# Kernel tuning notes

Measured on AMD Instinct MI355X. Metric: run time of the kernel, lower is better.

## Reference

```python
import jax, jax.numpy as jnp
import numpy as np

B, R, T, D = 16, 1024, 512, 1024
H = 1024  # hidden_dim

def setup_inputs() -> dict:
    key = jax.random.key(0)
    ks = jax.random.split(key, 8)
    s_in = 1.0 / np.sqrt(D)
    s_comb = 1.0 / np.sqrt(3 * D)
    return {
        "region_feats": jax.random.normal(ks[0], (B, R, D), jnp.float32),
        "query_embs": jax.random.normal(ks[1], (B, T, D), jnp.float32),
        "Wr": jax.random.normal(ks[2], (D, H), jnp.float32) * s_in,
        "br": jnp.zeros((H,), jnp.float32),
        "Wq": jax.random.normal(ks[3], (D, H), jnp.float32) * s_in,
        "bq": jnp.zeros((H,), jnp.float32),
        "Ws": jax.random.normal(ks[4], (3 * D, 1), jnp.float32) * s_comb,
        "bs": jnp.zeros((1,), jnp.float32),
    }

def reference(region_feats, query_embs, Wr, br, Wq, bq, Ws, bs):
    # Dense projections
    R_proj = region_feats @ Wr + br            # [B,R,H]
    Q_proj = query_embs @ Wq + bq              # [B,T,H]
    # Unscaled cross-attention scores
    scores = jnp.einsum('brd,btd->brt', R_proj, Q_proj)  # [B,R,T]
    attn = jax.nn.softmax(scores, axis=-1)
    # Attend over RAW query embeddings (as in source)
    attended = jnp.einsum('brt,btd->brd', attn, query_embs)  # [B,R,D]
    combined = jnp.concatenate(
        [region_feats, attended, region_feats * attended], axis=-1)  # [B,R,3D]
    out = combined @ Ws + bs                    # [B,R,1]
    return jnp.squeeze(out, axis=-1)            # [B,R]
```

## Files before the change

kernel.cpp:

```cpp
#include <hip/hip_runtime.h>


#define BD 16
#define RD 1024
#define TD 512
#define DD 1024
#define BR (BD * RD)

typedef _Float16 half8 __attribute__((ext_vector_type(8)));
typedef _Float16 half4 __attribute__((ext_vector_type(4)));
typedef float floatx4 __attribute__((ext_vector_type(4)));

__device__ __forceinline__ float wave_sum(float v) {
#pragma unroll
  for (int off = 32; off > 0; off >>= 1) v += __shfl_down(v, off);
  return v;
}

__device__ __forceinline__ half8 cvt8(float4 a, float4 b) {
  half8 h = {(_Float16)a.x, (_Float16)a.y, (_Float16)a.z, (_Float16)a.w,
             (_Float16)b.x, (_Float16)b.y, (_Float16)b.z, (_Float16)b.w};
  return h;
}

__device__ __forceinline__ void gl16(const _Float16* g, _Float16* l) {
  __builtin_amdgcn_global_load_lds(
      (const __attribute__((address_space(1))) void*)g,
      (__attribute__((address_space(3))) void*)l, 16, 0, 0);
}

#define VMW_(N) asm volatile("s_waitcnt vmcnt(" #N ")" ::: "memory")
#define VMW(N) VMW_(N)
#define BARR                        \
  __builtin_amdgcn_s_barrier();     \
  asm volatile("" ::: "memory")

__global__ __launch_bounds__(256) void prep_all(
    const float* __restrict__ Wr, const float* __restrict__ Wq,
    const float* __restrict__ Ws, const float* __restrict__ br,
    const float* __restrict__ region, const float* __restrict__ query,
    _Float16* __restrict__ M2, _Float16* __restrict__ Ws16,
    float* __restrict__ wqbr, _Float16* __restrict__ wqbr16,
    _Float16* __restrict__ r16, float* __restrict__ rdvec,
    _Float16* __restrict__ q16, float* __restrict__ h1) {
  __shared__ __align__(16) _Float16 lds[2 * 2 * 2048];
  const int blk = blockIdx.x, tid = threadIdx.x;

  if (blk < 256) {
    const int m0 = (blk >> 4) * 64, n0 = (blk & 15) * 64;
    const int lane = tid & 63, w = tid >> 6;
    const int wr = w >> 1, wc = w & 1;
    const int srow = tid >> 2, slot = tid & 3;
    const int scol = (slot ^ ((srow >> 1) & 3)) * 8;
    const long offA = (long)(m0 + srow) * DD + scol;
    const long offB = (long)(n0 + srow) * DD + scol;
    const int wofs = srow * 32 + slot * 8;
    const int NK = DD / 32;
    float4 a0, a1, b0, b1;
    a0 = *(const float4*)(Wr + offA); a1 = *(const float4*)(Wr + offA + 4);
    b0 = *(const float4*)(Wq + offB); b1 = *(const float4*)(Wq + offB + 4);
    *(int4*)&lds[wofs] = *(int4*)&(const half8&)cvt8(a0, a1);
    {
      half8 hb = cvt8(b0, b1);
      *(half8*)&lds[2048 + wofs] = hb;
    }
    a0 = *(const float4*)(Wr + offA + 32); a1 = *(const float4*)(Wr + offA + 36);
    b0 = *(const float4*)(Wq + offB + 32); b1 = *(const float4*)(Wq + offB + 36);
    __syncthreads();
    floatx4 acc[2][2] = {};
    const int fr = lane & 15, g = lane >> 4;
    const int fs = (g ^ ((fr >> 1) & 3)) * 8;
    for (int kt = 0; kt < NK; ++kt) {
      const int cur = (kt & 1) * 4096, nxt = ((kt + 1) & 1) * 4096;
      if (kt + 1 < NK) {
        half8 ha = cvt8(a0, a1), hb = cvt8(b0, b1);
        *(half8*)&lds[nxt + wofs] = ha;
        *(half8*)&lds[nxt + 2048 + wofs] = hb;
      }
      if (kt + 2 < NK) {
        const long go = (long)(kt + 2) * 32;
        a0 = *(const float4*)(Wr + offA + go); a1 = *(const float4*)(Wr + offA + go + 4);
        b0 = *(const float4*)(Wq + offB + go); b1 = *(const float4*)(Wq + offB + go + 4);
      }
      half8 af[2], bf[2];
#pragma unroll
      for (int i = 0; i < 2; ++i)
        af[i] = *(const half8*)&lds[cur + (32 * wr + 16 * i + fr) * 32 + fs];
#pragma unroll
      for (int j = 0; j < 2; ++j)
        bf[j] = *(const half8*)&lds[cur + 2048 + (32 * wc + 16 * j + fr) * 32 + fs];
#pragma unroll
      for (int i = 0; i < 2; ++i)
#pragma unroll
        for (int j = 0; j < 2; ++j)
          acc[i][j] = __builtin_amdgcn_mfma_f32_16x16x32_f16(af[i], bf[j], acc[i][j], 0, 0, 0);
      __syncthreads();
    }
    const int cr = g * 4, cc = fr;
#pragma unroll
    for (int i = 0; i < 2; ++i)
#pragma unroll
      for (int r = 0; r < 4; ++r)
#pragma unroll
        for (int j = 0; j < 2; ++j)
          M2[(long)(m0 + 32 * wr + 16 * i + cr + r) * DD + n0 + 32 * wc + 16 * j + cc] =
              (_Float16)acc[i][j][r];
  } else if (blk < 258) {
    const long i = (long)(blk - 256) * 1024 + tid * 4;
    const float4 v = *(const float4*)&Ws[DD + i];
    half4 h = {(_Float16)v.x, (_Float16)v.y, (_Float16)v.z, (_Float16)v.w};
    *(half4*)&Ws16[i] = h;
  } else if (blk < 514) {
    const int row = (blk - 258) * 4 + (tid >> 6);
    const int lane = tid & 63;
    const float* x = Wq + (long)row * DD;
    float s = 0.f;
    for (int k = lane; k < DD; k += 64) s += x[k] * br[k];
    s = wave_sum(s);
    if (lane == 0) {
      wqbr[row] = s;
      wqbr16[row] = (_Float16)s;
    }
  } else if (blk < 514 + BR / 4) {
    const int wid = tid >> 6, lane = tid & 63;
    const long row = (long)(blk - 514) * 4 + wid;
    const float* src = region + row * DD;
    _Float16* dst = r16 + row * DD;
    float rd = 0.f;
#pragma unroll
    for (int it = 0; it < 4; ++it) {
      const int c = it * 256 + lane * 4;
      const float4 v = *(const float4*)&src[c];
      const float4 w0 = *(const float4*)&Ws[c];
      half4 h = {(_Float16)v.x, (_Float16)v.y, (_Float16)v.z, (_Float16)v.w};
      *(half4*)&dst[c] = h;
      rd += v.x * w0.x + v.y * w0.y + v.z * w0.z + v.w * w0.w;
    }
    rd = wave_sum(rd);
    if (lane == 0) rdvec[row] = rd;
  } else {
    const int wid = tid >> 6, lane = tid & 63;
    const long row = (long)(blk - (514 + BR / 4)) * 4 + wid;
    const float* src = query + row * DD;
    _Float16* dst = q16 + row * DD;
    float hq = 0.f;
#pragma unroll
    for (int it = 0; it < 4; ++it) {
      const int c = it * 256 + lane * 4;
      const float4 v = *(const float4*)&src[c];
      const float4 w1 = *(const float4*)&Ws[DD + c];
      half4 h = {(_Float16)v.x, (_Float16)v.y, (_Float16)v.z, (_Float16)v.w};
      *(half4*)&dst[c] = h;
      hq += v.x * w1.x + v.y * w1.y + v.z * w1.z + v.w * w1.w;
    }
    hq = wave_sum(hq);
    if (lane == 0) h1[row] = hq;
  }
}

#define STAGE2(hh, sl)                                  \
  {                                                     \
    const long go_ = (long)(hh) * 32;                   \
    gl16(gA + go_, &lds[(sl) * 8192 + wbase]);          \
    gl16(gB + go_, &lds[(sl) * 8192 + 4096 + wbase]);   \
  }

#define COMP2(h, sl)                                                           \
  {                                                                            \
    half8 af[2], bf[4];                                                        \
    _Pragma("unroll") for (int i = 0; i < 2; ++i)                              \
      af[i] = *(const half8*)&lds[(sl) * 8192 + (32 * wr + 16 * i + fr) * 32 + fs]; \
    _Pragma("unroll") for (int j = 0; j < 4; ++j)                              \
      bf[j] = *(const half8*)&lds[(sl) * 8192 + 4096 + (64 * wc + 16 * j + fr) * 32 + fs]; \
    if (wc == 0) {                                                             \
      const half8 wb = *(const half8*)&wq_lds[(h) * 32 + g * 8];               \
      _Pragma("unroll") for (int i = 0; i < 2; ++i)                            \
        _Pragma("unroll") for (int e = 0; e < 8; ++e)                          \
          cvp[i] += (float)af[i][e] * (float)wb[e];                            \
    }                                                                          \
    __builtin_amdgcn_s_setprio(1);                                             \
    _Pragma("unroll") for (int i = 0; i < 2; ++i)                              \
      _Pragma("unroll") for (int j = 0; j < 4; ++j)                            \
        acc[i][j] = __builtin_amdgcn_mfma_f32_16x16x32_f16(af[i], bf[j], acc[i][j], 0, 0, 0); \
    __builtin_amdgcn_s_setprio(0);                                             \
  }

__global__ __launch_bounds__(512, 4) void qp_gemm(
    const _Float16* __restrict__ A, const _Float16* __restrict__ B,
    _Float16* __restrict__ C, const _Float16* __restrict__ wq16,
    float* __restrict__ cvec) {
  __shared__ __align__(16) _Float16 lds[4 * 8192];
  __shared__ __align__(16) _Float16 wq_lds[1024];
  const int lin = blockIdx.x;
  const int s = lin & 7, u = lin >> 3;
  const int mt = s * 8 + (u >> 3), nt = u & 7;
  const int m0 = mt * 128, n0 = nt * 128;
  const int tid = threadIdx.x, lane = tid & 63, w = tid >> 6;
  const int wr = w >> 1, wc = w & 1;

  const int lrow = lane >> 2, slot = lane & 3;
  const int scol = (slot ^ ((lrow >> 1) & 3)) * 8;
  const int srow = 16 * w + lrow;
  const _Float16* gA = A + (long)(m0 + srow) * DD + scol;
  const _Float16* gB = B + (long)(n0 + srow) * DD + scol;
  const int wbase = 512 * w;

  if (tid < 128) *(int4*)&wq_lds[tid * 8] = *(const int4*)&wq16[tid * 8];
  __syncthreads();

  floatx4 acc[2][4] = {};
  float cvp[2] = {0.f, 0.f};
  const int fr = lane & 15, g = lane >> 4;
  const int fs = (g ^ ((fr >> 1) & 3)) * 8;

  STAGE2(0, 0); STAGE2(1, 1); STAGE2(2, 2);
  VMW(4); BARR;

  for (int hb = 0; hb < 28; hb += 4) {
    STAGE2(hb + 3, 3); COMP2(hb + 0, 0); VMW(4); BARR;
    STAGE2(hb + 4, 0); COMP2(hb + 1, 1); VMW(4); BARR;
    STAGE2(hb + 5, 1); COMP2(hb + 2, 2); VMW(4); BARR;
    STAGE2(hb + 6, 2); COMP2(hb + 3, 3); VMW(4); BARR;
  }
  STAGE2(31, 3); COMP2(28, 0); VMW(4); BARR;
  COMP2(29, 1); VMW(2); BARR;
  COMP2(30, 2); VMW(0); BARR;
  COMP2(31, 3);

  if (wc == 0 && nt == 0) {
#pragma unroll
    for (int i = 0; i < 2; ++i) {
      float c = cvp[i];
      c += __shfl_xor(c, 16);
      c += __shfl_xor(c, 32);
      if (lane < 16) cvec[m0 + 32 * wr + 16 * i + lane] = c;
    }
  }

  const int cr = g * 4, cc = fr;
#pragma unroll
  for (int i = 0; i < 2; ++i)
#pragma unroll
    for (int r = 0; r < 4; ++r)
#pragma unroll
      for (int j = 0; j < 4; ++j)
        C[(long)(m0 + 32 * wr + 16 * i + cr + r) * DD + n0 + 64 * wc + 16 * j + cc] =
            (_Float16)acc[i][j][r];
}

__global__ __launch_bounds__(512, 4) void gemm_fused(
    const _Float16* __restrict__ A, const _Float16* __restrict__ B0,
    const _Float16* __restrict__ B1,
    float* __restrict__ Ms, float* __restrict__ Ls, float* __restrict__ Hs,
    const float* __restrict__ cvec, const float* __restrict__ h1,
    const _Float16* __restrict__ wsh, long sA, long sB) {
  __shared__ __align__(16) _Float16 lds[2 * 3 * 4096];
  __shared__ __align__(16) _Float16 wlds[1024];

  const int lin = blockIdx.x;
  const int s = lin & 7, u = lin >> 3;
  const int b = 2 * s + (u >> 5);
  const int t = u & 31;
  const int mt = t >> 2, nt = t & 3;
  const int m0 = mt * 128, n0 = nt * 128;
  A += (long)b * sA;
  B0 += (long)b * sB;
  B1 += (long)b * sB;

  const int tid = threadIdx.x, lane = tid & 63, w = tid >> 6;
  const int wr = w >> 2, wc = w & 3;

  const int lrow = lane >> 2, slot = lane & 3;
  const int scol = (slot ^ ((lrow >> 1) & 3)) * 8;
  const int srow = 16 * w + lrow;
  const _Float16* gA = A + (long)(m0 + srow) * DD + scol;
  const _Float16* gP = B0 + (long)(n0 + srow) * DD + scol;
  const _Float16* gQ = B1 + (long)(n0 + srow) * DD + scol;
  const int wbase = 512 * w;

  if (tid < 128) *(int4*)&wlds[tid * 8] = *(const int4*)&wsh[1024 + tid * 8];

  gl16(gA, &lds[wbase]);
  gl16(gP, &lds[4096 + wbase]);
  gl16(gQ, &lds[8192 + wbase]);
  __syncthreads();

  floatx4 accS[4][2] = {};
  floatx4 accH[4][2] = {};
  const int fr = lane & 15, g = lane >> 4;
  const int fs = (g ^ ((fr >> 1) & 3)) * 8;
  const int NK = DD / 32;

  for (int kt = 0; kt < NK; ++kt) {
    const int cur = (kt & 1) * 12288;
    const int nxt = cur ^ 12288;
    if (kt + 1 < NK) {
      const long go = (long)(kt + 1) * 32;
      gl16(gA + go, &lds[nxt + wbase]);
      gl16(gP + go, &lds[nxt + 4096 + wbase]);
      gl16(gQ + go, &lds[nxt + 8192 + wbase]);
    }
    half8 af[4], bp[2], bq[2];
#pragma unroll
    for (int i = 0; i < 4; ++i)
      af[i] = *(const half8*)&lds[cur + (64 * wr + 16 * i + fr) * 32 + fs];
#pragma unroll
    for (int j = 0; j < 2; ++j)
      bp[j] = *(const half8*)&lds[cur + 4096 + (32 * wc + 16 * j + fr) * 32 + fs];
#pragma unroll
    for (int j = 0; j < 2; ++j)
      bq[j] = *(const half8*)&lds[cur + 8192 + (32 * wc + 16 * j + fr) * 32 + fs];
    const half8 w2f = *(const half8*)&wlds[kt * 32 + g * 8];
#pragma unroll
    for (int j = 0; j < 2; ++j) bq[j] *= w2f;
#pragma unroll
    for (int i = 0; i < 4; ++i)
#pragma unroll
      for (int j = 0; j < 2; ++j)
        accS[i][j] = __builtin_amdgcn_mfma_f32_16x16x32_f16(af[i], bp[j], accS[i][j], 0, 0, 0);
#pragma unroll
    for (int i = 0; i < 4; ++i)
#pragma unroll
      for (int j = 0; j < 2; ++j)
        accH[i][j] = __builtin_amdgcn_mfma_f32_16x16x32_f16(af[i], bq[j], accH[i][j], 0, 0, 0);
    __syncthreads();
  }

  const int cr = g * 4, cc = fr;
  float cv[2], hv[2];
#pragma unroll
  for (int j = 0; j < 2; ++j) {
    const long col = (long)b * TD + n0 + 32 * wc + 16 * j + cc;
    cv[j] = cvec[col];
    hv[j] = h1[col];
  }

  float* smx = (float*)(void*)lds;
  float* slv = smx + 512;
  float* shv = slv + 512;
#pragma unroll
  for (int i = 0; i < 4; ++i) {
#pragma unroll
    for (int r = 0; r < 4; ++r) {
      float mx = fmaxf(accS[i][0][r] + cv[0], accS[i][1][r] + cv[1]);
      mx = fmaxf(mx, __shfl_xor(mx, 1));
      mx = fmaxf(mx, __shfl_xor(mx, 2));
      mx = fmaxf(mx, __shfl_xor(mx, 4));
      mx = fmaxf(mx, __shfl_xor(mx, 8));
      float l = 0.f, hs = 0.f;
#pragma unroll
      for (int j = 0; j < 2; ++j) {
        const float e = __expf(accS[i][j][r] + cv[j] - mx);
        l += e;
        hs += e * (accH[i][j][r] + hv[j]);
      }
      l += __shfl_xor(l, 1); hs += __shfl_xor(hs, 1);
      l += __shfl_xor(l, 2); hs += __shfl_xor(hs, 2);
      l += __shfl_xor(l, 4); hs += __shfl_xor(hs, 4);
      l += __shfl_xor(l, 8); hs += __shfl_xor(hs, 8);
      if (cc == 0) {
        const int rw = 16 * i + cr + r;
        smx[wr * 256 + wc * 64 + rw] = mx;
        slv[wr * 256 + wc * 64 + rw] = l;
        shv[wr * 256 + wc * 64 + rw] = hs;
      }
    }
  }
  __syncthreads();
  if (tid < 128) {
    const int rw = tid & 63, w2 = tid >> 6;
    float m4[4], gm = -1e30f;
#pragma unroll
    for (int c = 0; c < 4; ++c) {
      m4[c] = smx[w2 * 256 + c * 64 + rw];
      gm = fmaxf(gm, m4[c]);
    }
    float L = 0.f, H = 0.f;
#pragma unroll
    for (int c = 0; c < 4; ++c) {
      const float sc = __expf(m4[c] - gm);
      L += slv[w2 * 256 + c * 64 + rw] * sc;
      H += shv[w2 * 256 + c * 64 + rw] * sc;
    }
    const long gidx = (long)b * RD + m0 + 64 * w2 + rw;
    Ms[(long)nt * BR + gidx] = gm;
    Ls[(long)nt * BR + gidx] = L;
    Hs[(long)nt * BR + gidx] = H;
  }
}

__global__ __launch_bounds__(256) void combine(
    const float* __restrict__ Ms, const float* __restrict__ Ls,
    const float* __restrict__ Hs, const float* __restrict__ rdvec,
    const float* __restrict__ bs, float* __restrict__ out) {
  const int row = blockIdx.x * 256 + threadIdx.x;
  float mv[4];
  float gm = -1e30f;
#pragma unroll
  for (int c = 0; c < 4; ++c) {
    mv[c] = Ms[(long)c * BR + row];
    gm = fmaxf(gm, mv[c]);
  }
  float L = 0.f, HS = 0.f;
#pragma unroll
  for (int c = 0; c < 4; ++c) {
    const float sc = __expf(mv[c] - gm);
    L += Ls[(long)c * BR + row] * sc;
    HS += Hs[(long)c * BR + row] * sc;
  }
  out[row] = HS / L + rdvec[row] + bs[0];
}

extern "C" void kernel_launch(void* const* d_in, const int* in_sizes, int n_in,
                              void* d_out, int out_size, void* d_ws, size_t ws_size,
                              hipStream_t stream) {
  const float* region = (const float*)d_in[0];
  const float* query  = (const float*)d_in[1];
  const float* Wr     = (const float*)d_in[2];
  const float* br     = (const float*)d_in[3];
  const float* Wq     = (const float*)d_in[4];
  const float* Ws     = (const float*)d_in[6];
  const float* bs     = (const float*)d_in[7];
  float* out = (float*)d_out;

  char* p = (char*)d_ws;
  _Float16* region16 = (_Float16*)p;
  _Float16* query16  = (_Float16*)(p + (32u << 20));
  _Float16* Qp       = (_Float16*)(p + (48u << 20));
  _Float16* M2       = (_Float16*)(p + (64u << 20));
  _Float16* Ws16     = (_Float16*)(p + (66u << 20));
  float*    wqbr     = (float*)(p + (66u << 20) + 8192);
  _Float16* wqbr16   = (_Float16*)(p + (66u << 20) + 12288);
  float*    cvec     = (float*)(p + (66u << 20) + 16384);
  float*    rdvec    = (float*)(p + (66u << 20) + 65536);
  float*    h1       = (float*)(p + (66u << 20) + 131072);
  float*    Ms       = (float*)(p + (67u << 20));
  float*    Ls       = Ms + 4 * BR;
  float*    Hs       = Ls + 4 * BR;

  prep_all<<<dim3(514 + BR / 4 + BD * TD / 4), 256, 0, stream>>>(
      Wr, Wq, Ws, br, region, query, M2, Ws16, wqbr, wqbr16,
      region16, rdvec, query16, h1);
  qp_gemm<<<dim3(512), 512, 0, stream>>>(query16, M2, Qp, wqbr16, cvec);
  gemm_fused<<<dim3(512), 512, 0, stream>>>(
      region16, Qp, query16, Ms, Ls, Hs, cvec, h1, Ws16,
      (long)RD * DD, (long)TD * DD);
  combine<<<dim3(BR / 256), 256, 0, stream>>>(Ms, Ls, Hs, rdvec, bs, out);
}
```

Baseline: 217.9 us.

## Move region conversion into the Q-projection launch and simplify its GEMM pipeline

The region fp16 conversion and rdvec dot product, the h1 query dot product and the Ws16 conversion move out of the prep kernel into extra blocks of the Q-projection GEMM launch. The aim is to overlap this memory-bound work with the compute-bound GEMM and to shrink the prep kernel. The GEMM itself is rewritten from a 4-stage, explicit-waitcnt pipeline to a simpler double-buffered loop that reads wq16 straight from global memory, which may expose more load latency. The query rows are now read twice, once in prep_core for the fp16 copy and again for h1.

```diff
diff --git a/kernel.cpp b/kernel.cpp
--- a/kernel.cpp
+++ b/kernel.cpp
@@ -29,20 +29,11 @@
       (__attribute__((address_space(3))) void*)l, 16, 0, 0);
 }
 
-#define VMW_(N) asm volatile("s_waitcnt vmcnt(" #N ")" ::: "memory")
-#define VMW(N) VMW_(N)
-#define BARR                        \
-  __builtin_amdgcn_s_barrier();     \
-  asm volatile("" ::: "memory")
-
-__global__ __launch_bounds__(256) void prep_all(
+__global__ __launch_bounds__(256) void prep_core(
     const float* __restrict__ Wr, const float* __restrict__ Wq,
-    const float* __restrict__ Ws, const float* __restrict__ br,
-    const float* __restrict__ region, const float* __restrict__ query,
-    _Float16* __restrict__ M2, _Float16* __restrict__ Ws16,
-    float* __restrict__ wqbr, _Float16* __restrict__ wqbr16,
-    _Float16* __restrict__ r16, float* __restrict__ rdvec,
-    _Float16* __restrict__ q16, float* __restrict__ h1) {
+    const float* __restrict__ br, const float* __restrict__ query,
+    _Float16* __restrict__ M2, float* __restrict__ wqbr,
+    _Float16* __restrict__ wqbr16, _Float16* __restrict__ q16) {
   __shared__ __align__(16) _Float16 lds[2 * 2 * 2048];
   const int blk = blockIdx.x, tid = threadIdx.x;
 
@@ -105,13 +96,8 @@
         for (int j = 0; j < 2; ++j)
           M2[(long)(m0 + 32 * wr + 16 * i + cr + r) * DD + n0 + 32 * wc + 16 * j + cc] =
               (_Float16)acc[i][j][r];
-  } else if (blk < 258) {
-    const long i = (long)(blk - 256) * 1024 + tid * 4;
-    const float4 v = *(const float4*)&Ws[DD + i];
-    half4 h = {(_Float16)v.x, (_Float16)v.y, (_Float16)v.z, (_Float16)v.w};
-    *(half4*)&Ws16[i] = h;
-  } else if (blk < 514) {
-    const int row = (blk - 258) * 4 + (tid >> 6);
+  } else if (blk < 512) {
+    const int row = (blk - 256) * 4 + (tid >> 6);
     const int lane = tid & 63;
     const float* x = Wq + (long)row * DD;
     float s = 0.f;
@@ -121,111 +107,124 @@
       wqbr[row] = s;
       wqbr16[row] = (_Float16)s;
     }
-  } else if (blk < 514 + BR / 4) {
+  } else {
     const int wid = tid >> 6, lane = tid & 63;
-    const long row = (long)(blk - 514) * 4 + wid;
-    const float* src = region + row * DD;
-    _Float16* dst = r16 + row * DD;
-    float rd = 0.f;
+    const long row = (long)(blk - 512) * 4 + wid;
+    const float* src = query + row * DD;
+    _Float16* dst = q16 + row * DD;
 #pragma unroll
     for (int it = 0; it < 4; ++it) {
       const int c = it * 256 + lane * 4;
       const float4 v = *(const float4*)&src[c];
-      const float4 w0 = *(const float4*)&Ws[c];
       half4 h = {(_Float16)v.x, (_Float16)v.y, (_Float16)v.z, (_Float16)v.w};
       *(half4*)&dst[c] = h;
-      rd += v.x * w0.x + v.y * w0.y + v.z * w0.z + v.w * w0.w;
-    }
-    rd = wave_sum(rd);
-    if (lane == 0) rdvec[row] = rd;
-  } else {
+    }
+  }
+}
+
+__global__ __launch_bounds__(512, 4) void qp_plus(
+    const _Float16* __restrict__ A, const _Float16* __restrict__ Bm,
+    _Float16* __restrict__ C, const _Float16* __restrict__ wq16,
+    float* __restrict__ cvec, const float* __restrict__ region,
+    const float* __restrict__ Ws, _Float16* __restrict__ r16,
+    float* __restrict__ rdvec, const float* __restrict__ query,
+    float* __restrict__ h1, _Float16* __restrict__ Ws16) {
+  __shared__ __align__(16) _Float16 lds[2 * 2 * 4096];
+  const int blk = blockIdx.x, tid = threadIdx.x;
+
+  if (blk >= 512) {
     const int wid = tid >> 6, lane = tid & 63;
-    const long row = (long)(blk - (514 + BR / 4)) * 4 + wid;
-    const float* src = query + row * DD;
-    _Float16* dst = q16 + row * DD;
-    float hq = 0.f;
-#pragma unroll
-    for (int it = 0; it < 4; ++it) {
-      const int c = it * 256 + lane * 4;
-      const float4 v = *(const float4*)&src[c];
-      const float4 w1 = *(const float4*)&Ws[DD + c];
+    if (blk < 2560) {
+      const long row = (long)(blk - 512) * 8 + wid;
+      const float* src = region + row * DD;
+      _Float16* dst = r16 + row * DD;
+      float rd = 0.f;
+#pragma unroll
+      for (int it = 0; it < 4; ++it) {
+        const int c = it * 256 + lane * 4;
+        const float4 v = *(const float4*)&src[c];
+        const float4 w0 = *(const float4*)&Ws[c];
+        half4 h = {(_Float16)v.x, (_Float16)v.y, (_Float16)v.z, (_Float16)v.w};
+        *(half4*)&dst[c] = h;
+        rd += v.x * w0.x + v.y * w0.y + v.z * w0.z + v.w * w0.w;
+      }
+      rd = wave_sum(rd);
+      if (lane == 0) rdvec[row] = rd;
+    } else if (blk < 3584) {
+      const long row = (long)(blk - 2560) * 8 + wid;
+      const float* src = query + row * DD;
+      float hq = 0.f;
+#pragma unroll
+      for (int it = 0; it < 4; ++it) {
+        const int c = it * 256 + lane * 4;
+        const float4 v = *(const float4*)&src[c];
+        const float4 w1 = *(const float4*)&Ws[DD + c];
+        hq += v.x * w1.x + v.y * w1.y + v.z * w1.z + v.w * w1.w;
+      }
+      hq = wave_sum(hq);
+      if (lane == 0) h1[row] = hq;
+    } else {
+      const long i = (long)tid * 4;
+      const float4 v = *(const float4*)&Ws[DD + i];
       half4 h = {(_Float16)v.x, (_Float16)v.y, (_Float16)v.z, (_Float16)v.w};
-      *(half4*)&dst[c] = h;
-      hq += v.x * w1.x + v.y * w1.y + v.z * w1.z + v.w * w1.w;
-    }
-    hq = wave_sum(hq);
-    if (lane == 0) h1[row] = hq;
-  }
-}
-
-#define STAGE2(hh, sl)                                  \
-  {                                                     \
-    const long go_ = (long)(hh) * 32;                   \
-    gl16(gA + go_, &lds[(sl) * 8192 + wbase]);          \
-    gl16(gB + go_, &lds[(sl) * 8192 + 4096 + wbase]);   \
-  }
-
-#define COMP2(h, sl)                                                           \
-  {                                                                            \
-    half8 af[2], bf[4];                                                        \
-    _Pragma("unroll") for (int i = 0; i < 2; ++i)                              \
-      af[i] = *(const half8*)&lds[(sl) * 8192 + (32 * wr + 16 * i + fr) * 32 + fs]; \
-    _Pragma("unroll") for (int j = 0; j < 4; ++j)                              \
-      bf[j] = *(const half8*)&lds[(sl) * 8192 + 4096 + (64 * wc + 16 * j + fr) * 32 + fs]; \
-    if (wc == 0) {                                                             \
-      const half8 wb = *(const half8*)&wq_lds[(h) * 32 + g * 8];               \
-      _Pragma("unroll") for (int i = 0; i < 2; ++i)                            \
-        _Pragma("unroll") for (int e = 0; e < 8; ++e)                          \
-          cvp[i] += (float)af[i][e] * (float)wb[e];                            \
-    }                                                                          \
-    __builtin_amdgcn_s_setprio(1);                                             \
-    _Pragma("unroll") for (int i = 0; i < 2; ++i)                              \
-      _Pragma("unroll") for (int j = 0; j < 4; ++j)                            \
-        acc[i][j] = __builtin_amdgcn_mfma_f32_16x16x32_f16(af[i], bf[j], acc[i][j], 0, 0, 0); \
-    __builtin_amdgcn_s_setprio(0);                                             \
-  }
-
-__global__ __launch_bounds__(512, 4) void qp_gemm(
-    const _Float16* __restrict__ A, const _Float16* __restrict__ B,
-    _Float16* __restrict__ C, const _Float16* __restrict__ wq16,
-    float* __restrict__ cvec) {
-  __shared__ __align__(16) _Float16 lds[4 * 8192];
-  __shared__ __align__(16) _Float16 wq_lds[1024];
-  const int lin = blockIdx.x;
+      *(half4*)&Ws16[i] = h;
+    }
+    return;
+  }
+
+  const int lin = blk;
   const int s = lin & 7, u = lin >> 3;
   const int mt = s * 8 + (u >> 3), nt = u & 7;
   const int m0 = mt * 128, n0 = nt * 128;
-  const int tid = threadIdx.x, lane = tid & 63, w = tid >> 6;
+  const int lane = tid & 63, w = tid >> 6;
   const int wr = w >> 1, wc = w & 1;
 
   const int lrow = lane >> 2, slot = lane & 3;
   const int scol = (slot ^ ((lrow >> 1) & 3)) * 8;
   const int srow = 16 * w + lrow;
   const _Float16* gA = A + (long)(m0 + srow) * DD + scol;
-  const _Float16* gB = B + (long)(n0 + srow) * DD + scol;
+  const _Float16* gB = Bm + (long)(n0 + srow) * DD + scol;
   const int wbase = 512 * w;
 
-  if (tid < 128) *(int4*)&wq_lds[tid * 8] = *(const int4*)&wq16[tid * 8];
+  gl16(gA, &lds[wbase]);
+  gl16(gB, &lds[4096 + wbase]);
   __syncthreads();
 
   floatx4 acc[2][4] = {};
   float cvp[2] = {0.f, 0.f};
   const int fr = lane & 15, g = lane >> 4;
   const int fs = (g ^ ((fr >> 1) & 3)) * 8;
-
-  STAGE2(0, 0); STAGE2(1, 1); STAGE2(2, 2);
-  VMW(4); BARR;
-
-  for (int hb = 0; hb < 28; hb += 4) {
-    STAGE2(hb + 3, 3); COMP2(hb + 0, 0); VMW(4); BARR;
-    STAGE2(hb + 4, 0); COMP2(hb + 1, 1); VMW(4); BARR;
-    STAGE2(hb + 5, 1); COMP2(hb + 2, 2); VMW(4); BARR;
-    STAGE2(hb + 6, 2); COMP2(hb + 3, 3); VMW(4); BARR;
-  }
-  STAGE2(31, 3); COMP2(28, 0); VMW(4); BARR;
-  COMP2(29, 1); VMW(2); BARR;
-  COMP2(30, 2); VMW(0); BARR;
-  COMP2(31, 3);
+  const int NK = DD / 32;
+
+  for (int kt = 0; kt < NK; ++kt) {
+    const int cur = (kt & 1) * 8192, nxt = cur ^ 8192;
+    if (kt + 1 < NK) {
+      const long go = (long)(kt + 1) * 32;
+      gl16(gA + go, &lds[nxt + wbase]);
+      gl16(gB + go, &lds[nxt + 4096 + wbase]);
+    }
+    half8 af[2], bf[4];
+#pragma unroll
+    for (int i = 0; i < 2; ++i)
+      af[i] = *(const half8*)&lds[cur + (32 * wr + 16 * i + fr) * 32 + fs];
+#pragma unroll
+    for (int j = 0; j < 4; ++j)
+      bf[j] = *(const half8*)&lds[cur + 4096 + (64 * wc + 16 * j + fr) * 32 + fs];
+    if (wc == 0) {
+      const half8 wb = *(const half8*)&wq16[kt * 32 + g * 8];
+#pragma unroll
+      for (int i = 0; i < 2; ++i)
+#pragma unroll
+        for (int e = 0; e < 8; ++e)
+          cvp[i] += (float)af[i][e] * (float)wb[e];
+    }
+#pragma unroll
+    for (int i = 0; i < 2; ++i)
+#pragma unroll
+      for (int j = 0; j < 4; ++j)
+        acc[i][j] = __builtin_amdgcn_mfma_f32_16x16x32_f16(af[i], bf[j], acc[i][j], 0, 0, 0);
+    __syncthreads();
+  }
 
   if (wc == 0 && nt == 0) {
 #pragma unroll
@@ -438,10 +437,11 @@
   float*    Ls       = Ms + 4 * BR;
   float*    Hs       = Ls + 4 * BR;
 
-  prep_all<<<dim3(514 + BR / 4 + BD * TD / 4), 256, 0, stream>>>(
-      Wr, Wq, Ws, br, region, query, M2, Ws16, wqbr, wqbr16,
-      region16, rdvec, query16, h1);
-  qp_gemm<<<dim3(512), 512, 0, stream>>>(query16, M2, Qp, wqbr16, cvec);
+  prep_core<<<dim3(2560), 256, 0, stream>>>(
+      Wr, Wq, br, query, M2, wqbr, wqbr16, query16);
+  qp_plus<<<dim3(3585), 512, 0, stream>>>(
+      query16, M2, Qp, wqbr16, cvec, region, Ws, region16, rdvec,
+      query, h1, Ws16);
   gemm_fused<<<dim3(512), 512, 0, stream>>>(
       region16, Qp, query16, Ms, Ls, Hs, cvec, h1, Ws16,
       (long)RD * DD, (long)TD * DD);
```

Result: slower. 230.5 us (+5.8%).

## Replace 4-stage async GEMM pipeline with double-buffered 64-wide K tiles

Applied to the files above, without the earlier changes.

Rewrites the qp_gemm main loop. The old code used a 4-slot LDS ring with explicit vmcnt waits and raw barriers. The new code uses two LDS buffers of 64-wide K tiles, each filled by async global-to-LDS loads, with one __syncthreads per tile. It also drops the LDS staging of the wq16 vector, which is now read directly from global memory inside the loop, and removes the s_setprio hints around the MFMAs. The aim is fewer barriers and simpler synchronisation, at the cost of shallower prefetch depth and a full vmcnt drain at every barrier.

```diff
diff --git a/kernel.cpp b/kernel.cpp
--- a/kernel.cpp
+++ b/kernel.cpp
@@ -28,12 +28,6 @@
       (const __attribute__((address_space(1))) void*)g,
       (__attribute__((address_space(3))) void*)l, 16, 0, 0);
 }
-
-#define VMW_(N) asm volatile("s_waitcnt vmcnt(" #N ")" ::: "memory")
-#define VMW(N) VMW_(N)
-#define BARR                        \
-  __builtin_amdgcn_s_barrier();     \
-  asm volatile("" ::: "memory")
 
 __global__ __launch_bounds__(256) void prep_all(
     const float* __restrict__ Wr, const float* __restrict__ Wq,
@@ -158,39 +152,11 @@
   }
 }
 
-#define STAGE2(hh, sl)                                  \
-  {                                                     \
-    const long go_ = (long)(hh) * 32;                   \
-    gl16(gA + go_, &lds[(sl) * 8192 + wbase]);          \
-    gl16(gB + go_, &lds[(sl) * 8192 + 4096 + wbase]);   \
-  }
-
-#define COMP2(h, sl)                                                           \
-  {                                                                            \
-    half8 af[2], bf[4];                                                        \
-    _Pragma("unroll") for (int i = 0; i < 2; ++i)                              \
-      af[i] = *(const half8*)&lds[(sl) * 8192 + (32 * wr + 16 * i + fr) * 32 + fs]; \
-    _Pragma("unroll") for (int j = 0; j < 4; ++j)                              \
-      bf[j] = *(const half8*)&lds[(sl) * 8192 + 4096 + (64 * wc + 16 * j + fr) * 32 + fs]; \
-    if (wc == 0) {                                                             \
-      const half8 wb = *(const half8*)&wq_lds[(h) * 32 + g * 8];               \
-      _Pragma("unroll") for (int i = 0; i < 2; ++i)                            \
-        _Pragma("unroll") for (int e = 0; e < 8; ++e)                          \
-          cvp[i] += (float)af[i][e] * (float)wb[e];                            \
-    }                                                                          \
-    __builtin_amdgcn_s_setprio(1);                                             \
-    _Pragma("unroll") for (int i = 0; i < 2; ++i)                              \
-      _Pragma("unroll") for (int j = 0; j < 4; ++j)                            \
-        acc[i][j] = __builtin_amdgcn_mfma_f32_16x16x32_f16(af[i], bf[j], acc[i][j], 0, 0, 0); \
-    __builtin_amdgcn_s_setprio(0);                                             \
-  }
-
 __global__ __launch_bounds__(512, 4) void qp_gemm(
     const _Float16* __restrict__ A, const _Float16* __restrict__ B,
     _Float16* __restrict__ C, const _Float16* __restrict__ wq16,
     float* __restrict__ cvec) {
-  __shared__ __align__(16) _Float16 lds[4 * 8192];
-  __shared__ __align__(16) _Float16 wq_lds[1024];
+  __shared__ __align__(16) _Float16 lds[2 * 16384];
   const int lin = blockIdx.x;
   const int s = lin & 7, u = lin >> 3;
   const int mt = s * 8 + (u >> 3), nt = u & 7;
@@ -205,27 +171,52 @@
   const _Float16* gB = B + (long)(n0 + srow) * DD + scol;
   const int wbase = 512 * w;
 
-  if (tid < 128) *(int4*)&wq_lds[tid * 8] = *(const int4*)&wq16[tid * 8];
+  gl16(gA, &lds[wbase]);
+  gl16(gA + 32, &lds[4096 + wbase]);
+  gl16(gB, &lds[8192 + wbase]);
+  gl16(gB + 32, &lds[12288 + wbase]);
   __syncthreads();
 
   floatx4 acc[2][4] = {};
   float cvp[2] = {0.f, 0.f};
   const int fr = lane & 15, g = lane >> 4;
   const int fs = (g ^ ((fr >> 1) & 3)) * 8;
-
-  STAGE2(0, 0); STAGE2(1, 1); STAGE2(2, 2);
-  VMW(4); BARR;
-
-  for (int hb = 0; hb < 28; hb += 4) {
-    STAGE2(hb + 3, 3); COMP2(hb + 0, 0); VMW(4); BARR;
-    STAGE2(hb + 4, 0); COMP2(hb + 1, 1); VMW(4); BARR;
-    STAGE2(hb + 5, 1); COMP2(hb + 2, 2); VMW(4); BARR;
-    STAGE2(hb + 6, 2); COMP2(hb + 3, 3); VMW(4); BARR;
-  }
-  STAGE2(31, 3); COMP2(28, 0); VMW(4); BARR;
-  COMP2(29, 1); VMW(2); BARR;
-  COMP2(30, 2); VMW(0); BARR;
-  COMP2(31, 3);
+  const int NK2 = DD / 64;
+
+  for (int kt2 = 0; kt2 < NK2; ++kt2) {
+    const int cur = (kt2 & 1) * 16384, nxt = cur ^ 16384;
+    if (kt2 + 1 < NK2) {
+      const long go = (long)(kt2 + 1) * 64;
+      gl16(gA + go, &lds[nxt + wbase]);
+      gl16(gA + go + 32, &lds[nxt + 4096 + wbase]);
+      gl16(gB + go, &lds[nxt + 8192 + wbase]);
+      gl16(gB + go + 32, &lds[nxt + 12288 + wbase]);
+    }
+#pragma unroll
+    for (int ks = 0; ks < 2; ++ks) {
+      half8 af[2], bf[4];
+#pragma unroll
+      for (int i = 0; i < 2; ++i)
+        af[i] = *(const half8*)&lds[cur + ks * 4096 + (32 * wr + 16 * i + fr) * 32 + fs];
+#pragma unroll
+      for (int j = 0; j < 4; ++j)
+        bf[j] = *(const half8*)&lds[cur + 8192 + ks * 4096 + (64 * wc + 16 * j + fr) * 32 + fs];
+      if (wc == 0) {
+        const half8 wb = *(const half8*)&wq16[(2 * kt2 + ks) * 32 + g * 8];
+#pragma unroll
+        for (int i = 0; i < 2; ++i)
+#pragma unroll
+          for (int e = 0; e < 8; ++e)
+            cvp[i] += (float)af[i][e] * (float)wb[e];
+      }
+#pragma unroll
+      for (int i = 0; i < 2; ++i)
+#pragma unroll
+        for (int j = 0; j < 4; ++j)
+          acc[i][j] = __builtin_amdgcn_mfma_f32_16x16x32_f16(af[i], bf[j], acc[i][j], 0, 0, 0);
+    }
+    __syncthreads();
+  }
 
   if (wc == 0 && nt == 0) {
 #pragma unroll
```

After: 222.8 us. 1.02x slower.

## Fuse region fp32-to-fp16 conversion and Ws0 dot into main attention GEMM

Applied to the files above, without the earlier changes.

Drops the separate prep pass that converted region_feats to fp16 and computed the region·Ws[0:D] dot product. The fused GEMM now streams fp32 region tiles into LDS directly and converts them to fp16 in registers before the MFMAs. Blocks with nt==0 also accumulate the rdvec dot product from the same LDS tiles. This removes a 64MB fp32 read plus a 32MB fp16 write/read round trip. In exchange the A tile takes twice the LDS, each of the four N-tiles per row block re-reads region in fp32, and conversion work is added inside the inner loop, which may cut occupancy.

```diff
diff --git a/kernel.cpp b/kernel.cpp
--- a/kernel.cpp
+++ b/kernel.cpp
@@ -28,6 +28,11 @@
       (const __attribute__((address_space(1))) void*)g,
       (__attribute__((address_space(3))) void*)l, 16, 0, 0);
 }
+__device__ __forceinline__ void gl16b(const void* g, void* l) {
+  __builtin_amdgcn_global_load_lds(
+      (const __attribute__((address_space(1))) void*)g,
+      (__attribute__((address_space(3))) void*)l, 16, 0, 0);
+}
 
 #define VMW_(N) asm volatile("s_waitcnt vmcnt(" #N ")" ::: "memory")
 #define VMW(N) VMW_(N)
@@ -38,10 +43,9 @@
 __global__ __launch_bounds__(256) void prep_all(
     const float* __restrict__ Wr, const float* __restrict__ Wq,
     const float* __restrict__ Ws, const float* __restrict__ br,
-    const float* __restrict__ region, const float* __restrict__ query,
+    const float* __restrict__ query,
     _Float16* __restrict__ M2, _Float16* __restrict__ Ws16,
     float* __restrict__ wqbr, _Float16* __restrict__ wqbr16,
-    _Float16* __restrict__ r16, float* __restrict__ rdvec,
     _Float16* __restrict__ q16, float* __restrict__ h1) {
   __shared__ __align__(16) _Float16 lds[2 * 2 * 2048];
   const int blk = blockIdx.x, tid = threadIdx.x;
@@ -121,26 +125,9 @@
       wqbr[row] = s;
       wqbr16[row] = (_Float16)s;
     }
-  } else if (blk < 514 + BR / 4) {
+  } else {
     const int wid = tid >> 6, lane = tid & 63;
     const long row = (long)(blk - 514) * 4 + wid;
-    const float* src = region + row * DD;
-    _Float16* dst = r16 + row * DD;
-    float rd = 0.f;
-#pragma unroll
-    for (int it = 0; it < 4; ++it) {
-      const int c = it * 256 + lane * 4;
-      const float4 v = *(const float4*)&src[c];
-      const float4 w0 = *(const float4*)&Ws[c];
-      half4 h = {(_Float16)v.x, (_Float16)v.y, (_Float16)v.z, (_Float16)v.w};
-      *(half4*)&dst[c] = h;
-      rd += v.x * w0.x + v.y * w0.y + v.z * w0.z + v.w * w0.w;
-    }
-    rd = wave_sum(rd);
-    if (lane == 0) rdvec[row] = rd;
-  } else {
-    const int wid = tid >> 6, lane = tid & 63;
-    const long row = (long)(blk - (514 + BR / 4)) * 4 + wid;
     const float* src = query + row * DD;
     _Float16* dst = q16 + row * DD;
     float hq = 0.f;
@@ -249,13 +236,15 @@
 }
 
 __global__ __launch_bounds__(512, 4) void gemm_fused(
-    const _Float16* __restrict__ A, const _Float16* __restrict__ B0,
+    const float* __restrict__ Af, const _Float16* __restrict__ B0,
     const _Float16* __restrict__ B1,
     float* __restrict__ Ms, float* __restrict__ Ls, float* __restrict__ Hs,
     const float* __restrict__ cvec, const float* __restrict__ h1,
-    const _Float16* __restrict__ wsh, long sA, long sB) {
-  __shared__ __align__(16) _Float16 lds[2 * 3 * 4096];
+    const _Float16* __restrict__ wsh, const float* __restrict__ ws0,
+    float* __restrict__ rdvec, long sA, long sB) {
+  __shared__ __align__(16) char ldsb[2 * 32768];
   __shared__ __align__(16) _Float16 wlds[1024];
+  __shared__ __align__(16) float ws0l[1024];
 
   const int lin = blockIdx.x;
   const int s = lin & 7, u = lin >> 3;
@@ -263,7 +252,7 @@
   const int t = u & 31;
   const int mt = t >> 2, nt = t & 3;
   const int m0 = mt * 128, n0 = nt * 128;
-  A += (long)b * sA;
+  const float* Ab = Af + (long)b * sA;
   B0 += (long)b * sB;
   B1 += (long)b * sB;
 
@@ -273,46 +262,65 @@
   const int lrow = lane >> 2, slot = lane & 3;
   const int scol = (slot ^ ((lrow >> 1) & 3)) * 8;
   const int srow = 16 * w + lrow;
-  const _Float16* gA = A + (long)(m0 + srow) * DD + scol;
+  const float*    gA = Ab + (long)(m0 + srow) * DD + scol;
   const _Float16* gP = B0 + (long)(n0 + srow) * DD + scol;
   const _Float16* gQ = B1 + (long)(n0 + srow) * DD + scol;
-  const int wbase = 512 * w;
+  const int wB = 1024 * w;
 
   if (tid < 128) *(int4*)&wlds[tid * 8] = *(const int4*)&wsh[1024 + tid * 8];
-
-  gl16(gA, &lds[wbase]);
-  gl16(gP, &lds[4096 + wbase]);
-  gl16(gQ, &lds[8192 + wbase]);
+  if (tid >= 256) *(float4*)&ws0l[(tid - 256) * 4] = *(const float4*)&ws0[(tid - 256) * 4];
+
+  gl16b(gA,     ldsb + wB);
+  gl16b(gA + 4, ldsb + 8192 + wB);
+  gl16b(gP,     ldsb + 16384 + wB);
+  gl16b(gQ,     ldsb + 24576 + wB);
   __syncthreads();
 
   floatx4 accS[4][2] = {};
   floatx4 accH[4][2] = {};
+  float rdp = 0.f;
   const int fr = lane & 15, g = lane >> 4;
-  const int fs = (g ^ ((fr >> 1) & 3)) * 8;
+  const int fs2 = (g ^ ((fr >> 1) & 3)) * 16;
+  const bool doRd = (nt == 0);
+  const int rr = tid >> 2, c4 = tid & 3;
+  const int sR = c4 ^ ((rr >> 1) & 3);
   const int NK = DD / 32;
 
   for (int kt = 0; kt < NK; ++kt) {
-    const int cur = (kt & 1) * 12288;
-    const int nxt = cur ^ 12288;
+    const int cur = (kt & 1) * 32768;
+    const int nxt = cur ^ 32768;
     if (kt + 1 < NK) {
       const long go = (long)(kt + 1) * 32;
-      gl16(gA + go, &lds[nxt + wbase]);
-      gl16(gP + go, &lds[nxt + 4096 + wbase]);
-      gl16(gQ + go, &lds[nxt + 8192 + wbase]);
+      gl16b(gA + go,     ldsb + nxt + wB);
+      gl16b(gA + go + 4, ldsb + nxt + 8192 + wB);
+      gl16b(gP + go,     ldsb + nxt + 16384 + wB);
+      gl16b(gQ + go,     ldsb + nxt + 24576 + wB);
     }
     half8 af[4], bp[2], bq[2];
 #pragma unroll
-    for (int i = 0; i < 4; ++i)
-      af[i] = *(const half8*)&lds[cur + (64 * wr + 16 * i + fr) * 32 + fs];
+    for (int i = 0; i < 4; ++i) {
+      const int rA = 64 * wr + 16 * i + fr;
+      const float4 lo = *(const float4*)&ldsb[cur + rA * 64 + fs2];
+      const float4 hi = *(const float4*)&ldsb[cur + 8192 + rA * 64 + fs2];
+      af[i] = cvt8(lo, hi);
+    }
 #pragma unroll
     for (int j = 0; j < 2; ++j)
-      bp[j] = *(const half8*)&lds[cur + 4096 + (32 * wc + 16 * j + fr) * 32 + fs];
+      bp[j] = *(const half8*)&ldsb[cur + 16384 + (32 * wc + 16 * j + fr) * 64 + fs2];
 #pragma unroll
     for (int j = 0; j < 2; ++j)
-      bq[j] = *(const half8*)&lds[cur + 8192 + (32 * wc + 16 * j + fr) * 32 + fs];
+      bq[j] = *(const half8*)&ldsb[cur + 24576 + (32 * wc + 16 * j + fr) * 64 + fs2];
+    if (doRd) {
+      const float4 alo = *(const float4*)&ldsb[cur + rr * 64 + sR * 16];
+      const float4 ahi = *(const float4*)&ldsb[cur + 8192 + rr * 64 + sR * 16];
+      const float4 wlo = *(const float4*)&ws0l[kt * 32 + c4 * 8];
+      const float4 whi = *(const float4*)&ws0l[kt * 32 + c4 * 8 + 4];
+      rdp += alo.x * wlo.x + alo.y * wlo.y + alo.z * wlo.z + alo.w * wlo.w +
+             ahi.x * whi.x + ahi.y * whi.y + ahi.z * whi.z + ahi.w * whi.w;
+    }
     const half8 w2f = *(const half8*)&wlds[kt * 32 + g * 8];
-#pragma unroll
-    for (int j = 0; j < 2; ++j) bq[j] *= w2f;
+    bq[0] *= w2f;
+    bq[1] *= w2f;
 #pragma unroll
     for (int i = 0; i < 4; ++i)
 #pragma unroll
@@ -324,6 +332,13 @@
       for (int j = 0; j < 2; ++j)
         accH[i][j] = __builtin_amdgcn_mfma_f32_16x16x32_f16(af[i], bq[j], accH[i][j], 0, 0, 0);
     __syncthreads();
+  }
+
+  if (doRd) {
+    float rv = rdp;
+    rv += __shfl_xor(rv, 1);
+    rv += __shfl_xor(rv, 2);
+    if (c4 == 0) rdvec[(long)b * RD + m0 + rr] = rv;
   }
 
   const int cr = g * 4, cc = fr;
@@ -335,7 +350,7 @@
     hv[j] = h1[col];
   }
 
-  float* smx = (float*)(void*)lds;
+  float* smx = (float*)(void*)ldsb;
   float* slv = smx + 512;
   float* shv = slv + 512;
 #pragma unroll
@@ -424,7 +439,6 @@
   float* out = (float*)d_out;
 
   char* p = (char*)d_ws;
-  _Float16* region16 = (_Float16*)p;
   _Float16* query16  = (_Float16*)(p + (32u << 20));
   _Float16* Qp       = (_Float16*)(p + (48u << 20));
   _Float16* M2       = (_Float16*)(p + (64u << 20));
@@ -438,12 +452,11 @@
   float*    Ls       = Ms + 4 * BR;
   float*    Hs       = Ls + 4 * BR;
 
-  prep_all<<<dim3(514 + BR / 4 + BD * TD / 4), 256, 0, stream>>>(
-      Wr, Wq, Ws, br, region, query, M2, Ws16, wqbr, wqbr16,
-      region16, rdvec, query16, h1);
+  prep_all<<<dim3(514 + BD * TD / 4), 256, 0, stream>>>(
+      Wr, Wq, Ws, br, query, M2, Ws16, wqbr, wqbr16, query16, h1);
   qp_gemm<<<dim3(512), 512, 0, stream>>>(query16, M2, Qp, wqbr16, cvec);
   gemm_fused<<<dim3(512), 512, 0, stream>>>(
-      region16, Qp, query16, Ms, Ls, Hs, cvec, h1, Ws16,
+      region, Qp, query16, Ms, Ls, Hs, cvec, h1, Ws16, Ws, rdvec,
       (long)RD * DD, (long)TD * DD);
   combine<<<dim3(BR / 256), 256, 0, stream>>>(Ms, Ls, Hs, rdvec, bs, out);
 }
```

Measured after the change: 384.9 us. 1.77x slower.
